# Optimization experiments

Measured on AMD Instinct MI355X. Metric: run time of the kernel, lower is better.

Reference implementation:

```python
import jax, jax.numpy as jnp
import numpy as np

# ---------------- Wigner-D machinery (real basis, e3nn conventions) ----------------

def _change_basis_real_to_complex(l):
    q = np.zeros((2*l+1, 2*l+1), dtype=np.complex128)
    for m in range(-l, 0):
        q[l+m, l+abs(m)] = 1/np.sqrt(2)
        q[l+m, l-abs(m)] = -1j/np.sqrt(2)
    q[l, l] = 1.0
    for m in range(1, l+1):
        q[l+m, l+abs(m)] = (-1)**m / np.sqrt(2)
        q[l+m, l-abs(m)] = 1j*(-1)**m / np.sqrt(2)
    return (-1j)**l * q

def _so3_generators(l):
    m = np.arange(-l, l)
    raising = np.diag(-np.sqrt(l*(l+1) - m*(m+1)), k=-1).astype(np.complex128)
    m = np.arange(-l+1, l+1)
    lowering = np.diag(np.sqrt(l*(l+1) - m*(m-1)), k=1).astype(np.complex128)
    m = np.arange(-l, l+1)
    Xs = [0.5*(raising+lowering), np.diag(1j*m), -0.5j*(raising-lowering)]
    Q = _change_basis_real_to_complex(l)
    return [np.real(np.conj(Q.T) @ X @ Q) for X in Xs]

def _expm_batch(A, t):
    # exp(t_n * A) for real antisymmetric A, via eigendecomposition
    w, V = np.linalg.eig(A.astype(np.complex128))
    Vinv = np.linalg.inv(V)
    E = np.exp(np.outer(t, w))  # [n, d]
    return np.real(np.einsum('ij,nj,jk->nik', V, E, Vinv))

def _wigner_D(l, alpha, beta, gamma):
    X = _so3_generators(l)
    return _expm_batch(X[1], alpha) @ _expm_batch(X[0], beta) @ _expm_batch(X[1], gamma)

def _flat_wigner(lmax, a, b, c):
    return np.concatenate([np.sqrt(2*l+1) * _wigner_D(l, a, b, c).reshape(len(a), -1)
                           for l in range(lmax+1)], axis=-1)

def _sh_alpha_beta(lmax, a, b):
    z = np.zeros_like(a)
    return np.concatenate([np.sqrt(2*l+1) * _wigner_D(l, a, b, z)[:, :, l]
                           for l in range(lmax+1)], axis=-1)

# ---------------- grids ----------------

def _so3_near_identity_grid(max_beta=np.pi/8, max_gamma=2*np.pi, n_alpha=8, n_beta=3, n_gamma=8):
    beta = np.arange(1, n_beta+1) * max_beta / n_beta
    alpha = np.linspace(0, 2*np.pi, n_alpha, endpoint=False)
    pre_gamma = np.linspace(-max_gamma, max_gamma, n_gamma)
    A, B, C = np.meshgrid(alpha, beta, pre_gamma, indexing='ij')
    return A.ravel(), B.ravel(), (C - A).ravel()

def _s2_near_identity_grid(max_beta=np.pi/8, n_alpha=8, n_beta=3):
    beta = np.arange(1, n_beta+1) * max_beta / n_beta
    alpha = np.linspace(0, 2*np.pi, n_alpha, endpoint=False)
    A, B = np.meshgrid(alpha, beta, indexing='ij')
    return A.ravel(), B.ravel()

def _so3_full_grid(res):
    a = 2*np.pi*np.arange(2*res)/(2*res)
    b = (np.arange(2*res)+0.5)*np.pi/(2*res)
    A, B, C = np.meshgrid(a, b, a, indexing='ij')
    qw = np.sin(B.ravel()); qw = qw / qw.sum()
    return A.ravel(), B.ravel(), C.ravel(), qw

# ---------------- constants for lmax=[6,4,4,2], feat=[32,64,128,128], N=8 ----------------
RES = 8
_ga, _gb, _gc = _so3_near_identity_grid()
D_K = jnp.asarray(_flat_wigner(4, _ga, _gb, _gc), jnp.float32)      # [192, 165] kernel basis
_fa, _fb, _fc, _qw = _so3_full_grid(RES)
D_ACT = jnp.asarray(_flat_wigner(4, _fa, _fb, _fc), jnp.float32)    # [4096, 165] act grid
QW = jnp.asarray(_qw, jnp.float32)                                   # [4096] quadrature
_sa, _sb = _s2_near_identity_grid()
Y_S2 = jnp.asarray(_sh_alpha_beta(2, _sa, _sb), jnp.float32)        # [24, 9]

# ---------------- layers ----------------

def _so3_linear(x, psi, lmax_in, lmax_out):
    # x: [B, f_in, sum_{l<=lmax_in}(2l+1)^2]; psi: [f_in, f_out, sum_{l<=lmin}(2l+1)^2]
    B, f_in, _ = x.shape
    f_out = psi.shape[1]
    lmin = min(lmax_in, lmax_out)
    outs, ox, op = [], 0, 0
    for l in range(lmax_out + 1):
        d = 2*l + 1
        if l <= lmin:
            xl = x[:, :, ox:ox + d*d].reshape(B, f_in, d, d)
            pl = psi[:, :, op:op + d*d].reshape(f_in, f_out, d, d)
            ol = jnp.einsum('xyuv,bxum->byvm', pl, xl) / np.sqrt(f_in * d)
            outs.append(ol.reshape(B, f_out, d*d))
            ox += d*d; op += d*d
        else:
            outs.append(jnp.zeros((B, f_out, d*d), x.dtype))
    return jnp.concatenate(outs, axis=-1)

def _so3_to_s2(x, psi, lmax_in, lmax_out):
    B, f_in, _ = x.shape
    f_out = psi.shape[1]
    lmin = min(lmax_in, lmax_out)
    outs, ox, op = [], 0, 0
    for l in range(lmax_out + 1):
        d = 2*l + 1
        if l <= lmin:
            xl = x[:, :, ox:ox + d*d].reshape(B, f_in, d, d)
            pl = psi[:, :, op:op + d].reshape(f_in, f_out, d)
            outs.append(jnp.einsum('xyu,bxum->bym', pl, xl) / np.sqrt(f_in * d))
            ox += d*d; op += d
        else:
            outs.append(jnp.zeros((B, f_out, d), x.dtype))
    return jnp.concatenate(outs, axis=-1)

def _so3_act(x):
    # SO3 Fourier -> grid signal, pointwise relu (2nd-moment normalized), grid -> Fourier
    s = jnp.einsum('ni,bfi->bfn', D_ACT, x)          # [B, f, 4096]
    s = np.sqrt(2.0) * jax.nn.relu(s)                 # normalize2mom(relu)
    return jnp.einsum('ni,bfn->bfi', D_ACT * QW[:, None], s)

def _forward(x, w0, w1, w_lin):
    n_k = D_K.shape[0]
    psi0 = jnp.einsum('ni,xyn->xyi', D_K, w0) / n_k   # [32, 64, 165]
    x = _so3_linear(x, psi0, 6, 4)
    x = _so3_act(x)
    psi1 = jnp.einsum('ni,xyn->xyi', D_K, w1) / n_k   # [64, 128, 165]
    x = _so3_linear(x, psi1, 4, 4)
    x = _so3_act(x)
    psi2 = jnp.einsum('ni,xyn->xyi', Y_S2, w_lin) / Y_S2.shape[0]  # [128, 128, 9]
    return _so3_to_s2(x, psi2, 4, 2)                  # [B, 128, 9]

# ---------------- harness ----------------

def setup_inputs() -> dict:
    key = jax.random.key(0)
    k1, k2, k3, k4 = jax.random.split(key, 4)
    return {
        'x': jax.random.normal(k1, (64, 32, 455), jnp.float32),
        'w0': jax.random.normal(k2, (32, 64, 192), jnp.float32),
        'w1': jax.random.normal(k3, (64, 128, 192), jnp.float32),
        'w_lin': jax.random.normal(k4, (128, 128, 24), jnp.float32),
    }

def reference(x, w0, w1, w_lin):
    return _forward(x, w0, w1, w_lin)
```

## Files before the change

kernel.cpp:

```cpp
#include <hip/hip_runtime.h>
#include <cmath>
#include <complex>
#include <cstring>
#include <vector>

#ifndef M_PI
#define M_PI 3.14159265358979323846
#endif

namespace wig {

using cplx = std::complex<double>;

static void matmul(const double* A, const double* B, double* C, int d) {
    for (int i = 0; i < d; ++i)
        for (int j = 0; j < d; ++j) {
            double s = 0;
            for (int k = 0; k < d; ++k) s += A[i*d+k]*B[k*d+j];
            C[i*d+j] = s;
        }
}

struct Gen { std::vector<double> X0, X1; int d; };

static Gen make_gen(int l) {
    int d = 2*l+1;
    std::vector<cplx> rais(d*d, cplx(0,0)), low(d*d, cplx(0,0));
    for (int i = 0; i+1 < d; ++i) {
        double m = -l + i;
        rais[(i+1)*d + i] = cplx(-std::sqrt(l*(l+1.0) - m*(m+1.0)), 0.0);
    }
    for (int i = 0; i+1 < d; ++i) {
        double m = -l + 1 + i;
        low[i*d + (i+1)] = cplx(std::sqrt(l*(l+1.0) - m*(m-1.0)), 0.0);
    }
    std::vector<cplx> Xc0(d*d, cplx(0,0)), Xc1(d*d, cplx(0,0));
    for (int i = 0; i < d*d; ++i) Xc0[i] = 0.5*(rais[i] + low[i]);
    for (int i = 0; i < d; ++i) Xc1[i*d+i] = cplx(0.0, (double)(-l + i));
    std::vector<cplx> q(d*d, cplx(0,0));
    double is2 = 1.0/std::sqrt(2.0);
    for (int m = -l; m < 0; ++m) {
        q[(l+m)*d + (l-m)] = cplx(is2, 0);
        q[(l+m)*d + (l+m)] = cplx(0, -is2);
    }
    q[l*d + l] = cplx(1,0);
    for (int m = 1; m <= l; ++m) {
        double sgn = (m & 1) ? -1.0 : 1.0;
        q[(l+m)*d + (l+m)] = cplx(sgn*is2, 0);
        q[(l+m)*d + (l-m)] = cplx(0, sgn*is2);
    }
    cplx f;
    switch (l & 3) { case 0: f = cplx(1,0); break; case 1: f = cplx(0,-1); break;
                     case 2: f = cplx(-1,0); break; default: f = cplx(0,1); break; }
    for (auto& v : q) v *= f;
    Gen g; g.d = d; g.X0.assign(d*d, 0.0); g.X1.assign(d*d, 0.0);
    const std::vector<cplx>* Xs[2] = {&Xc0, &Xc1};
    std::vector<double>* Xr[2] = {&g.X0, &g.X1};
    for (int a = 0; a < 2; ++a) {
        std::vector<cplx> t1(d*d, cplx(0,0)), t2(d*d, cplx(0,0));
        for (int i = 0; i < d; ++i)
            for (int k = 0; k < d; ++k) {
                cplx x = (*Xs[a])[i*d+k];
                if (x == cplx(0,0)) continue;
                for (int j = 0; j < d; ++j) t1[i*d+j] += x*q[k*d+j];
            }
        for (int k = 0; k < d; ++k)
            for (int i = 0; i < d; ++i) {
                cplx qc = std::conj(q[k*d+i]);
                if (qc == cplx(0,0)) continue;
                for (int j = 0; j < d; ++j) t2[i*d+j] += qc*t1[k*d+j];
            }
        for (int i = 0; i < d*d; ++i) (*Xr[a])[i] = t2[i].real();
    }
    return g;
}

static std::vector<double> expm_t(const std::vector<double>& A, int d, double t) {
    std::vector<double> M(d*d);
    for (int i = 0; i < d*d; ++i) M[i] = A[i]*t;
    double nrm = 0;
    for (int i = 0; i < d; ++i) {
        double rs = 0;
        for (int j = 0; j < d; ++j) rs += std::fabs(M[i*d+j]);
        if (rs > nrm) nrm = rs;
    }
    int sq = 0;
    while (nrm > 0.5) { nrm *= 0.5; ++sq; }
    double sc = std::ldexp(1.0, -sq);
    for (auto& v : M) v *= sc;
    std::vector<double> R(d*d, 0.0), T(d*d, 0.0), tmp(d*d);
    for (int i = 0; i < d; ++i) { R[i*d+i] = 1.0; T[i*d+i] = 1.0; }
    for (int k = 1; k <= 26; ++k) {
        matmul(T.data(), M.data(), tmp.data(), d);
        double inv = 1.0/(double)k;
        for (int i = 0; i < d*d; ++i) { T[i] = tmp[i]*inv; R[i] += T[i]; }
    }
    for (int s = 0; s < sq; ++s) { matmul(R.data(), R.data(), tmp.data(), d); R = tmp; }
    return R;
}

static std::vector<double> wigD(const Gen& g, double a, double b, double c) {
    auto Ea = expm_t(g.X1, g.d, a);
    auto Eb = expm_t(g.X0, g.d, b);
    auto Ec = expm_t(g.X1, g.d, c);
    std::vector<double> t(g.d*g.d), r(g.d*g.d);
    matmul(Ea.data(), Eb.data(), t.data(), g.d);
    matmul(t.data(), Ec.data(), r.data(), g.d);
    return r;
}

}

static inline unsigned short f2bf_h(float f) {
    unsigned u; std::memcpy(&u, &f, 4);
    unsigned r = (u + 0x7FFFu + ((u >> 16) & 1u)) >> 16;
    return (unsigned short)r;
}
static inline float bf2f_h(unsigned short s) {
    unsigned u = ((unsigned)s) << 16; float f; std::memcpy(&f, &u, 4); return f;
}
__device__ __forceinline__ unsigned short f2bf_d(float f) {
    unsigned u = __float_as_uint(f);
    return (unsigned short)((u + 0x7FFFu + ((u >> 16) & 1u)) >> 16);
}
__device__ __forceinline__ float bf2f_d(unsigned short s) {
    return __uint_as_float(((unsigned)s) << 16);
}

typedef short short8 __attribute__((ext_vector_type(8)));
typedef float f32x4 __attribute__((ext_vector_type(4)));

#define GLOAD_LDS16(g, l) \
    __builtin_amdgcn_global_load_lds( \
        (const __attribute__((address_space(1))) unsigned int*)(g), \
        (__attribute__((address_space(3))) unsigned int*)(l), 16, 0, 0)

static float*          g_QW   = nullptr;
static float*          g_YS2  = nullptr;
static unsigned short* g_DKS  = nullptr;
static unsigned short* g_B1   = nullptr;
static unsigned short* g_B2T  = nullptr;
static float*          g_scratch = nullptr;

static const size_t WS_OFF   = 0;
static const size_t AP_OFF   = WS_OFF + 2359296;
static const size_t BP_OFF   = AP_OFF + 1013760;
static const size_t A1_OFF   = BP_OFF + 2027520;
static const size_t GH_OFF   = A1_OFF + 2359296;
static const size_t GL_OFF   = GH_OFF + 16777216;
static const size_t PP_OFF   = GL_OFF + 16777216;
static const size_t ZB_OFF   = PP_OFF + 12582912;
static const size_t PSI2_OFF = ZB_OFF + 1572864;
static const size_t TOTAL_F  = PSI2_OFF + 147456;

namespace {
struct InitCtx {
    InitCtx() {
        using namespace wig;
        Gen gens[5];
        for (int l = 0; l <= 4; ++l) gens[l] = make_gen(l);
        const int loff[5] = {0, 1, 10, 35, 84};

        double alpha8[8], beta3[3], preg8[8];
        for (int i = 0; i < 8; ++i) alpha8[i] = 2.0*M_PI*i/8.0;
        for (int i = 0; i < 3; ++i) beta3[i] = (i+1)*(M_PI/8.0)/3.0;
        for (int i = 0; i < 8; ++i) preg8[i] = -2.0*M_PI + i*(4.0*M_PI/7.0);
        std::vector<float> hDK((size_t)192*165);
        for (int ia = 0; ia < 8; ++ia)
        for (int ib = 0; ib < 3; ++ib)
        for (int ic = 0; ic < 8; ++ic) {
            int n = ia*24 + ib*8 + ic;
            double a = alpha8[ia], b = beta3[ib], c = preg8[ic] - alpha8[ia];
            for (int l = 0; l <= 4; ++l) {
                int d = 2*l+1;
                auto Dl = wigD(gens[l], a, b, c);
                double s = std::sqrt(2.0*l+1.0);
                for (int e = 0; e < d*d; ++e)
                    hDK[(size_t)n*165 + loff[l] + e] = (float)(s*Dl[e]);
            }
        }

        double ag[16], bg[16];
        for (int i = 0; i < 16; ++i) ag[i] = 2.0*M_PI*i/16.0;
        for (int i = 0; i < 16; ++i) bg[i] = (i+0.5)*M_PI/16.0;
        std::vector<std::vector<double>> Ea[5], Eb[5];
        for (int l = 0; l <= 4; ++l) {
            Ea[l].resize(16); Eb[l].resize(16);
            for (int i = 0; i < 16; ++i) {
                Ea[l][i] = expm_t(gens[l].X1, gens[l].d, ag[i]);
                Eb[l][i] = expm_t(gens[l].X0, gens[l].d, bg[i]);
            }
        }
        double qsum = 0;
        for (int ib = 0; ib < 16; ++ib) qsum += std::sin(bg[ib]);
        qsum *= 256.0;
        std::vector<float> hDA((size_t)4096*165), hQW(4096);
        for (int ia = 0; ia < 16; ++ia)
        for (int ib = 0; ib < 16; ++ib) {
            for (int ic = 0; ic < 16; ++ic)
                hQW[ia*256 + ib*16 + ic] = (float)(std::sin(bg[ib]) / qsum);
            for (int l = 0; l <= 4; ++l) {
                int d = gens[l].d;
                std::vector<double> tAB((size_t)d*d), r((size_t)d*d);
                matmul(Ea[l][ia].data(), Eb[l][ib].data(), tAB.data(), d);
                double s = std::sqrt(2.0*l+1.0);
                for (int ic = 0; ic < 16; ++ic) {
                    int n = ia*256 + ib*16 + ic;
                    matmul(tAB.data(), Ea[l][ic].data(), r.data(), d);
                    for (int e = 0; e < d*d; ++e)
                        hDA[(size_t)n*165 + loff[l] + e] = (float)(s*r[e]);
                }
            }
        }

        const int l2off[3] = {0, 1, 4};
        std::vector<float> hY((size_t)24*9);
        for (int ia = 0; ia < 8; ++ia)
        for (int ib = 0; ib < 3; ++ib) {
            int n = ia*3 + ib;
            for (int l = 0; l <= 2; ++l) {
                int d = 2*l+1;
                auto Dl = wigD(gens[l], alpha8[ia], beta3[ib], 0.0);
                double s = std::sqrt(2.0*l+1.0);
                for (int u = 0; u < d; ++u)
                    hY[(size_t)n*9 + l2off[l] + u] = (float)(s*Dl[u*d + l]);
            }
        }

        std::vector<unsigned short> hDKS((size_t)192*576, 0);
        for (int i = 0; i < 165; ++i)
            for (int k = 0; k < 192; ++k) {
                float f = hDK[(size_t)k*165 + i];
                unsigned short h = f2bf_h(f);
                unsigned short lo = f2bf_h(f - bf2f_h(h));
                hDKS[(size_t)i*576 + k]       = h;
                hDKS[(size_t)i*576 + 192 + k] = lo;
                hDKS[(size_t)i*576 + 384 + k] = h;
            }

        std::vector<unsigned short> Dh((size_t)4096*192, 0), Dl2((size_t)4096*192, 0);
        for (int n = 0; n < 4096; ++n)
            for (int i = 0; i < 165; ++i) {
                float f = hDA[(size_t)n*165 + i];
                unsigned short h = f2bf_h(f);
                Dh[(size_t)n*192 + i] = h;
                Dl2[(size_t)n*192 + i] = f2bf_h(f - bf2f_h(h));
            }
        std::vector<unsigned short> hB1((size_t)4096*576);
        for (int n = 0; n < 4096; ++n)
            for (int j = 0; j < 192; ++j) {
                hB1[(size_t)n*576 + j]       = Dh[(size_t)n*192 + j];
                hB1[(size_t)n*576 + 192 + j] = Dl2[(size_t)n*192 + j];
                hB1[(size_t)n*576 + 384 + j] = Dh[(size_t)n*192 + j];
            }
        std::vector<unsigned short> hB2T((size_t)192*12288);
        for (int j = 0; j < 192; ++j)
            for (int k = 0; k < 4096; ++k) {
                hB2T[(size_t)j*12288 + k]        = Dh[(size_t)k*192 + j];
                hB2T[(size_t)j*12288 + 4096 + k] = Dl2[(size_t)k*192 + j];
                hB2T[(size_t)j*12288 + 8192 + k] = Dh[(size_t)k*192 + j];
            }

        (void)hipMalloc((void**)&g_QW,  hQW.size()*sizeof(float));
        (void)hipMalloc((void**)&g_YS2, hY.size()*sizeof(float));
        (void)hipMalloc((void**)&g_DKS, hDKS.size()*sizeof(unsigned short));
        (void)hipMalloc((void**)&g_B1,  hB1.size()*sizeof(unsigned short));
        (void)hipMalloc((void**)&g_B2T, hB2T.size()*sizeof(unsigned short));
        (void)hipMalloc((void**)&g_scratch, TOTAL_F*sizeof(float));
        (void)hipMemcpy(g_QW,  hQW.data(),  hQW.size()*sizeof(float),  hipMemcpyHostToDevice);
        (void)hipMemcpy(g_YS2, hY.data(),   hY.size()*sizeof(float),   hipMemcpyHostToDevice);
        (void)hipMemcpy(g_DKS, hDKS.data(), hDKS.size()*sizeof(unsigned short), hipMemcpyHostToDevice);
        (void)hipMemcpy(g_B1,  hB1.data(),  hB1.size()*sizeof(unsigned short),  hipMemcpyHostToDevice);
        (void)hipMemcpy(g_B2T, hB2T.data(), hB2T.size()*sizeof(unsigned short), hipMemcpyHostToDevice);
    }
};
static InitCtx g_init_ctx;
}

struct PsiArgs {
    const unsigned short* A;
    const unsigned short* B;
    unsigned short* O;
    int boff[5], kp[5];
    int fout;
};
struct APackArgs {
    const float* X;
    unsigned short* O;
    int cum[6];
    int aoff[5], kp[5], kl[5];
    int bs, fs, total;
};
struct LinArgs {
    const unsigned short* A;
    const unsigned short* B;
    unsigned short* O;
    int cum[6];
    int aoff[5], boff[5], kp[5];
    float rs[5];
    int fout;
};

__device__ __constant__ int c_loff[5] = {0, 1, 10, 35, 84};

__device__ __forceinline__ int swz_src8(int c) { return ((c ^ (c >> 3)) & 7) * 8; }


__global__ __launch_bounds__(256) void sph_psi2_kernel(
        const float* __restrict__ wl, const float* __restrict__ Y,
        float* __restrict__ psi2) {
    __shared__ float Ys[216];
    int tid = threadIdx.x;
    if (tid < 216) Ys[tid] = Y[tid];
    __syncthreads();
    int o = blockIdx.x*256 + tid;
    const float* w = wl + (size_t)o*24;
    float wv[24];
    #pragma unroll
    for (int k = 0; k < 24; k += 4) {
        f32x4 v = *(const f32x4*)&w[k];
        wv[k] = v[0]; wv[k+1] = v[1]; wv[k+2] = v[2]; wv[k+3] = v[3];
    }
    float acc[9] = {};
    #pragma unroll
    for (int k = 0; k < 24; ++k)
        #pragma unroll
        for (int i = 0; i < 9; ++i)
            acc[i] += wv[k] * Ys[k*9 + i];
    float* po = psi2 + (size_t)o*9;
    #pragma unroll
    for (int i = 0; i < 9; ++i) po[i] = acc[i] * (1.0f/24.0f);
}

__global__ __launch_bounds__(64) void sph_s2_wave(
        const float* __restrict__ z, const float* __restrict__ psi2,
        float* __restrict__ out) {
    int blk = blockIdx.x;
    int b = blk >> 7, y = blk & 127;
    int lane = threadIdx.x;
    float acc[9] = {};
    #pragma unroll
    for (int xi = 0; xi < 2; ++xi) {
        int x = lane + xi*64;
        const float* zr = z + (size_t)(b*128 + x)*192;
        const float* pr = psi2 + (size_t)(x*128 + y)*9;
        float p[9];
        #pragma unroll
        for (int i = 0; i < 9; ++i) p[i] = pr[i];
        acc[0] += p[0] * zr[0];
        #pragma unroll
        for (int u = 0; u < 3; ++u)
            #pragma unroll
            for (int m = 0; m < 3; ++m)
                acc[1+m] += p[1+u] * zr[1 + u*3 + m];
        #pragma unroll
        for (int u = 0; u < 5; ++u)
            #pragma unroll
            for (int m = 0; m < 5; ++m)
                acc[4+m] += p[4+u] * zr[10 + u*5 + m];
    }
    #pragma unroll
    for (int i = 0; i < 9; ++i) {
        float v = acc[i];
        #pragma unroll
        for (int off = 32; off > 0; off >>= 1)
            v += __shfl_down(v, off, 64);
        acc[i] = v;
    }
    if (lane == 0) {
        float* po = out + (size_t)blk*9;
        const float s0 = 0.0883883476483184406f;
        const float s1 = 0.0510310363079828938f;
        const float s2 = 0.0395284707521047416f;
        po[0] = acc[0] * s0;
        po[1] = acc[1] * s1; po[2] = acc[2] * s1; po[3] = acc[3] * s1;
        po[4] = acc[4] * s2; po[5] = acc[5] * s2; po[6] = acc[6] * s2;
        po[7] = acc[7] * s2; po[8] = acc[8] * s2;
    }
}

__global__ void sph_wpack_kernel(const float* __restrict__ w, unsigned short* __restrict__ o, int total) {
    int t = blockIdx.x*blockDim.x + threadIdx.x;
    if (t >= total) return;
    int row = t / 192, k = t % 192;
    float v = w[t];
    unsigned short hi = f2bf_d(v);
    unsigned short lo = f2bf_d(v - bf2f_d(hi));
    size_t b = (size_t)row*576 + k;
    o[b] = hi; o[b+192] = hi; o[b+384] = lo;
}

__global__ void sph_apack_kernel(APackArgs ar) {
    int t = blockIdx.x*blockDim.x + threadIdx.x;
    if (t >= ar.total) return;
    int l = 0;
    #pragma unroll
    for (int i = 1; i < 5; ++i) if (t >= ar.cum[i]) l = i;
    int e = t - ar.cum[l];
    int d = 2*l + 1;
    int K = ar.kl[l];
    int row = e / K, k = e % K;
    int b = row / d, m = row % d;
    int x = k / d, u = k % d;
    float v = ar.X[(size_t)b*ar.bs + (size_t)x*ar.fs + c_loff[l] + u*d + m];
    unsigned short hi = f2bf_d(v);
    unsigned short lo = f2bf_d(v - bf2f_d(hi));
    int kp = ar.kp[l];
    size_t base = (size_t)ar.aoff[l] + (size_t)row*(3*kp);
    ar.O[base + k] = hi; ar.O[base + kp + k] = hi; ar.O[base + 2*kp + k] = lo;
}

__global__ void sph_reduce_kernel(const float* __restrict__ Pp, float* __restrict__ z, int P) {
    int o = blockIdx.x*blockDim.x + threadIdx.x;
    if (o >= P*192) return;
    float s = 0.f;
    for (int zz = 0; zz < 8; ++zz) s += Pp[(size_t)zz*P*192 + o];
    z[o] = s;
}

__global__ __launch_bounds__(256) void sph_psi_mfma(PsiArgs ar, int M) {
    __shared__ __align__(16) unsigned short As[64*64];
    __shared__ __align__(16) unsigned short Bs[64*64];
    int tid = threadIdx.x, lane = tid & 63, wid = tid >> 6;
    int l15 = lane & 15, l4 = lane >> 4;
    int sw = l15 & 7;
    int bm = blockIdx.x * 64, bn = blockIdx.y * 64;
    f32x4 acc[4] = {};
    for (int k0 = 0; k0 < 576; k0 += 64) {
        #pragma unroll
        for (int i = 0; i < 2; ++i) {
            int c = tid + i*256;
            int row = c >> 3, kb = swz_src8(c);
            GLOAD_LDS16(ar.A + (size_t)(bm + row)*576 + k0 + kb, As + c*8);
            GLOAD_LDS16(ar.B + (size_t)(bn + row)*576 + k0 + kb, Bs + c*8);
        }
        __syncthreads();
        #pragma unroll
        for (int ks = 0; ks < 2; ++ks) {
            int cs = ((ks*4 + l4) ^ sw) * 8;
            short8 av = *(const short8*)&As[(wid*16 + l15)*64 + cs];
            #pragma unroll
            for (int nj = 0; nj < 4; ++nj) {
                short8 bv = *(const short8*)&Bs[(nj*16 + l15)*64 + cs];
                acc[nj] = __builtin_amdgcn_mfma_f32_16x16x32_bf16(av, bv, acc[nj], 0, 0, 0);
            }
        }
        __syncthreads();
    }
    #pragma unroll
    for (int nj = 0; nj < 4; ++nj) {
        int i = bn + nj*16 + l15;
        if (i >= 165) continue;
        int l, st;
        if (i < 1)       { l = 0; st = 0;  }
        else if (i < 10) { l = 1; st = 1;  }
        else if (i < 35) { l = 2; st = 10; }
        else if (i < 84) { l = 3; st = 35; }
        else             { l = 4; st = 84; }
        int d = 2*l + 1;
        int w = i - st;
        int u = w / d, v = w % d;
        int kp = ar.kp[l];
        #pragma unroll
        for (int r = 0; r < 4; ++r) {
            int R = bm + wid*16 + l4*4 + r;
            int x = R / ar.fout, y = R % ar.fout;
            float val = acc[nj][r] * (1.0f/192.0f);
            unsigned short hi = f2bf_d(val);
            unsigned short lo = f2bf_d(val - bf2f_d(hi));
            size_t base = (size_t)ar.boff[l] + (size_t)(y*d + v)*(3*kp) + (x*d + u);
            ar.O[base] = hi; ar.O[base + kp] = lo; ar.O[base + 2*kp] = hi;
        }
    }
}

__global__ __launch_bounds__(256) void sph_lin_mfma(LinArgs ar) {
    int bid = blockIdx.x;
    int l = 0;
    #pragma unroll
    for (int i = 1; i < 5; ++i) if (bid >= ar.cum[i]) l = i;
    int t = bid - ar.cum[l];
    int d = 2*l + 1;
    int NB = (ar.fout >> 6) * d;
    int tm = t / NB, tn = t % NB;
    int K3 = 3 * ar.kp[l];
    const unsigned short* Ab = ar.A + ar.aoff[l] + (size_t)tm*64*K3;
    const unsigned short* Bb = ar.B + ar.boff[l] + (size_t)tn*64*K3;
    __shared__ __align__(16) unsigned short As[64*64];
    __shared__ __align__(16) unsigned short Bs[64*64];
    int tid = threadIdx.x, lane = tid & 63, wid = tid >> 6;
    int l15 = lane & 15, l4 = lane >> 4;
    int sw = l15 & 7;
    f32x4 acc[4] = {};
    for (int k0 = 0; k0 < K3; k0 += 64) {
        #pragma unroll
        for (int i = 0; i < 2; ++i) {
            int c = tid + i*256;
            int row = c >> 3, kb = swz_src8(c);
            GLOAD_LDS16(Ab + (size_t)row*K3 + k0 + kb, As + c*8);
            GLOAD_LDS16(Bb + (size_t)row*K3 + k0 + kb, Bs + c*8);
        }
        __syncthreads();
        #pragma unroll
        for (int ks = 0; ks < 2; ++ks) {
            int cs = ((ks*4 + l4) ^ sw) * 8;
            short8 av = *(const short8*)&As[(wid*16 + l15)*64 + cs];
            #pragma unroll
            for (int nj = 0; nj < 4; ++nj) {
                short8 bv = *(const short8*)&Bs[(nj*16 + l15)*64 + cs];
                acc[nj] = __builtin_amdgcn_mfma_f32_16x16x32_bf16(av, bv, acc[nj], 0, 0, 0);
            }
        }
        __syncthreads();
    }
    float rs = ar.rs[l];
    #pragma unroll
    for (int nj = 0; nj < 4; ++nj) {
        int col = tn*64 + nj*16 + l15;
        int y = col / d, v = col % d;
        #pragma unroll
        for (int r = 0; r < 4; ++r) {
            int row = tm*64 + wid*16 + l4*4 + r;
            int b = row / d, m = row % d;
            float val = acc[nj][r] * rs;
            unsigned short hi = f2bf_d(val);
            unsigned short lo = f2bf_d(val - bf2f_d(hi));
            size_t p = (size_t)(b*ar.fout + y)*576 + c_loff[l] + v*d + m;
            ar.O[p] = hi; ar.O[p + 192] = hi; ar.O[p + 384] = lo;
        }
    }
}

__global__ __launch_bounds__(256) void sph_gemm1_mfma(
        const unsigned short* __restrict__ A, const unsigned short* __restrict__ B,
        const float* __restrict__ qw,
        unsigned short* __restrict__ Gh, unsigned short* __restrict__ Gl, int M) {
    constexpr int K = 576;
    __shared__ __align__(16) unsigned short As[128*64];
    __shared__ __align__(16) unsigned short Bs[128*64];
    int tid = threadIdx.x;
    int lane = tid & 63, wid = tid >> 6;
    int wm = wid >> 1, wn = wid & 1;
    int bm = blockIdx.x * 128, bn = blockIdx.y * 128;
    int l15 = lane & 15, l4 = lane >> 4;
    int sw = l15 & 7;
    f32x4 acc[4][4] = {};
    for (int k0 = 0; k0 < K; k0 += 64) {
        #pragma unroll
        for (int i = 0; i < 4; ++i) {
            int c = tid + i*256;
            int row = c >> 3, kb = swz_src8(c);
            GLOAD_LDS16(A + (size_t)(bm + row)*K + k0 + kb, As + c*8);
            GLOAD_LDS16(B + (size_t)(bn + row)*K + k0 + kb, Bs + c*8);
        }
        __syncthreads();
        #pragma unroll
        for (int ks = 0; ks < 2; ++ks) {
            int cs = ((ks*4 + l4) ^ sw) * 8;
            short8 av[4], bv[4];
            #pragma unroll
            for (int mi = 0; mi < 4; ++mi)
                av[mi] = *(const short8*)&As[(wm*64 + mi*16 + l15)*64 + cs];
            #pragma unroll
            for (int nj = 0; nj < 4; ++nj)
                bv[nj] = *(const short8*)&Bs[(wn*64 + nj*16 + l15)*64 + cs];
            #pragma unroll
            for (int mi = 0; mi < 4; ++mi)
                #pragma unroll
                for (int nj = 0; nj < 4; ++nj)
                    acc[mi][nj] = __builtin_amdgcn_mfma_f32_16x16x32_bf16(av[mi], bv[nj], acc[mi][nj], 0, 0, 0);
        }
        __syncthreads();
    }
    const float SQ2 = 1.41421356237309515f;
    #pragma unroll
    for (int mi = 0; mi < 4; ++mi) {
        #pragma unroll
        for (int nj = 0; nj < 4; ++nj) {
            int col = bn + wn*64 + nj*16 + l15;
            float q = qw[col] * SQ2;
            #pragma unroll
            for (int r = 0; r < 4; ++r) {
                int row = bm + wm*64 + mi*16 + l4*4 + r;
                float g = fmaxf(acc[mi][nj][r], 0.f) * q;
                unsigned short hi = f2bf_d(g);
                unsigned short lo = f2bf_d(g - bf2f_d(hi));
                size_t idx = (size_t)row*4096 + col;
                Gh[idx] = hi; Gl[idx] = lo;
            }
        }
    }
}

__global__ __launch_bounds__(256) void sph_gemm2_mfma(
        const unsigned short* __restrict__ Gh, const unsigned short* __restrict__ Gl,
        const unsigned short* __restrict__ B, float* __restrict__ Pp, int M) {
    __shared__ __align__(16) unsigned short As[128*64];
    __shared__ __align__(16) unsigned short Bs[64*64];
    int tid = threadIdx.x;
    int lane = tid & 63, wid = tid >> 6;
    int wm = wid >> 1, wn = wid & 1;
    int bm = blockIdx.x * 128, bn = blockIdx.y * 64;
    int zc = blockIdx.z;
    int l15 = lane & 15, l4 = lane >> 4;
    int sw = l15 & 7;
    f32x4 acc[4][2] = {};
    for (int t = 0; t < 24; ++t) {
        int kg = zc*1536 + t*64;
        int seg = kg >> 12;
        const unsigned short* Abase = (seg == 2) ? Gl : Gh;
        int koff = kg & 4095;
        #pragma unroll
        for (int i = 0; i < 4; ++i) {
            int c = tid + i*256;
            int row = c >> 3, kb = swz_src8(c);
            GLOAD_LDS16(Abase + (size_t)(bm + row)*4096 + koff + kb, As + c*8);
        }
        #pragma unroll
        for (int i = 0; i < 2; ++i) {
            int c = tid + i*256;
            int row = c >> 3, kb = swz_src8(c);
            GLOAD_LDS16(B + (size_t)(bn + row)*12288 + kg + kb, Bs + c*8);
        }
        __syncthreads();
        #pragma unroll
        for (int ks = 0; ks < 2; ++ks) {
            int cs = ((ks*4 + l4) ^ sw) * 8;
            short8 av[4], bv[2];
            #pragma unroll
            for (int mi = 0; mi < 4; ++mi)
                av[mi] = *(const short8*)&As[(wm*64 + mi*16 + l15)*64 + cs];
            #pragma unroll
            for (int nj = 0; nj < 2; ++nj)
                bv[nj] = *(const short8*)&Bs[(wn*32 + nj*16 + l15)*64 + cs];
            #pragma unroll
            for (int mi = 0; mi < 4; ++mi)
                #pragma unroll
                for (int nj = 0; nj < 2; ++nj)
                    acc[mi][nj] = __builtin_amdgcn_mfma_f32_16x16x32_bf16(av[mi], bv[nj], acc[mi][nj], 0, 0, 0);
        }
        __syncthreads();
    }
    #pragma unroll
    for (int mi = 0; mi < 4; ++mi)
        #pragma unroll
        for (int nj = 0; nj < 2; ++nj) {
            int col = bn + wn*32 + nj*16 + l15;
            #pragma unroll
            for (int r = 0; r < 4; ++r) {
                int row = bm + wm*64 + mi*16 + l4*4 + r;
                Pp[((size_t)zc*M + row)*192 + col] = acc[mi][nj][r];
            }
        }
}

extern "C" void kernel_launch(void* const* d_in, const int* in_sizes, int n_in,
                              void* d_out, int out_size, void* d_ws, size_t ws_size,
                              hipStream_t stream) {
    const float* x  = (const float*)d_in[0];
    const float* w0 = (const float*)d_in[1];
    const float* w1 = (const float*)d_in[2];
    const float* wl = (const float*)d_in[3];
    float* out = (float*)d_out;

    unsigned short* Wsplit = (unsigned short*)(g_scratch + WS_OFF);
    unsigned short* Apack  = (unsigned short*)(g_scratch + AP_OFF);
    unsigned short* Bpack  = (unsigned short*)(g_scratch + BP_OFF);
    unsigned short* A1     = (unsigned short*)(g_scratch + A1_OFF);
    unsigned short* Gh     = (unsigned short*)(g_scratch + GH_OFF);
    unsigned short* Gl     = (unsigned short*)(g_scratch + GL_OFF);
    float* Pp   = g_scratch + PP_OFF;
    float* zbuf = g_scratch + ZB_OFF;
    float* psi2 = g_scratch + PSI2_OFF;

    (void)hipMemsetAsync(g_scratch + AP_OFF, 0, (1013760 + 2027520 + 2359296)*sizeof(float), stream);

    PsiArgs ps0; APackArgs ap0; LinArgs ln0;
    {
        const int kp[5]   = {64, 128, 192, 256, 320};
        const int kl[5]   = {32, 96, 160, 224, 288};
        const int aoff[5] = {0, 12288, 86016, 270336, 614400};
        const int cumT[6] = {0, 1, 10, 35, 84, 165};
        const int cumE[6] = {0, 2048, 20480, 71680, 172032, 337920};
        ps0.A = Wsplit; ps0.B = g_DKS; ps0.O = Bpack; ps0.fout = 64;
        ap0.X = x; ap0.O = Apack; ap0.bs = 32*455; ap0.fs = 455; ap0.total = 337920;
        ln0.A = Apack; ln0.B = Bpack; ln0.O = A1; ln0.fout = 64;
        for (int l = 0; l < 5; ++l) {
            ps0.boff[l] = aoff[l]; ps0.kp[l] = kp[l];
            ap0.aoff[l] = aoff[l]; ap0.kp[l] = kp[l]; ap0.kl[l] = kl[l];
            ln0.aoff[l] = aoff[l]; ln0.boff[l] = aoff[l]; ln0.kp[l] = kp[l];
            ln0.rs[l] = 1.0f/sqrtf(32.0f*(2*l+1));
        }
        for (int i = 0; i < 6; ++i) { ap0.cum[i] = cumE[i]; ln0.cum[i] = cumT[i]; }
    }
    PsiArgs ps1; APackArgs ap1; LinArgs ln1;
    {
        const int kp[5]   = {64, 192, 320, 448, 576};
        const int aoff[5] = {0, 12288, 122880, 430080, 1032192};
        const int boff[5] = {0, 24576, 245760, 860160, 2064384};
        const int cumT[6] = {0, 2, 20, 70, 168, 330};
        const int cumE[6] = {0, 4096, 40960, 143360, 344064, 675840};
        ps1.A = Wsplit; ps1.B = g_DKS; ps1.O = Bpack; ps1.fout = 128;
        ap1.X = zbuf; ap1.O = Apack; ap1.bs = 64*192; ap1.fs = 192; ap1.total = 675840;
        ln1.A = Apack; ln1.B = Bpack; ln1.O = A1; ln1.fout = 128;
        for (int l = 0; l < 5; ++l) {
            ps1.boff[l] = boff[l]; ps1.kp[l] = kp[l];
            ap1.aoff[l] = aoff[l]; ap1.kp[l] = kp[l]; ap1.kl[l] = kp[l];
            ln1.aoff[l] = aoff[l]; ln1.boff[l] = boff[l]; ln1.kp[l] = kp[l];
            ln1.rs[l] = 1.0f/sqrtf(64.0f*(2*l+1));
        }
        for (int i = 0; i < 6; ++i) { ap1.cum[i] = cumE[i]; ln1.cum[i] = cumT[i]; }
    }

    sph_wpack_kernel<<<(2048*192 + 255)/256, 256, 0, stream>>>(w0, Wsplit, 2048*192);
    sph_psi_mfma<<<dim3(2048/64, 3), 256, 0, stream>>>(ps0, 2048);
    sph_apack_kernel<<<(337920 + 255)/256, 256, 0, stream>>>(ap0);
    sph_lin_mfma<<<165, 256, 0, stream>>>(ln0);
    sph_gemm1_mfma<<<dim3(4096/128, 4096/128), 256, 0, stream>>>(A1, g_B1, g_QW, Gh, Gl, 4096);
    sph_gemm2_mfma<<<dim3(4096/128, 3, 8), 256, 0, stream>>>(Gh, Gl, g_B2T, Pp, 4096);
    sph_reduce_kernel<<<(4096*192 + 255)/256, 256, 0, stream>>>(Pp, zbuf, 4096);
    sph_wpack_kernel<<<(8192*192 + 255)/256, 256, 0, stream>>>(w1, Wsplit, 8192*192);
    sph_psi_mfma<<<dim3(8192/64, 3), 256, 0, stream>>>(ps1, 8192);
    sph_apack_kernel<<<(675840 + 255)/256, 256, 0, stream>>>(ap1);
    sph_lin_mfma<<<330, 256, 0, stream>>>(ln1);
    sph_gemm1_mfma<<<dim3(8192/128, 4096/128), 256, 0, stream>>>(A1, g_B1, g_QW, Gh, Gl, 8192);
    sph_gemm2_mfma<<<dim3(8192/128, 3, 8), 256, 0, stream>>>(Gh, Gl, g_B2T, Pp, 8192);
    sph_reduce_kernel<<<(8192*192 + 255)/256, 256, 0, stream>>>(Pp, zbuf, 8192);
    sph_psi2_kernel<<<64, 256, 0, stream>>>(wl, g_YS2, psi2);
    sph_s2_wave<<<8192, 64, 0, stream>>>(zbuf, psi2, out);
}
```

Before: 441.1 us.

## Fuse S2 activation GEMMs keeping ReLU intermediate in shared memory

Result: slower. 874.6 us (+98.3%).

```diff
diff --git a/kernel.cpp b/kernel.cpp
--- a/kernel.cpp
+++ b/kernel.cpp
@@ -531,127 +531,116 @@
     }
 }
 
-__global__ __launch_bounds__(256) void sph_gemm1_mfma(
-        const unsigned short* __restrict__ A, const unsigned short* __restrict__ B,
-        const float* __restrict__ qw,
-        unsigned short* __restrict__ Gh, unsigned short* __restrict__ Gl, int M) {
-    constexpr int K = 576;
+__global__ __launch_bounds__(256) void sph_act_fused(
+        const unsigned short* __restrict__ A1, const unsigned short* __restrict__ B1,
+        const unsigned short* __restrict__ B2T, const float* __restrict__ qw,
+        float* __restrict__ Pp, int M) {
     __shared__ __align__(16) unsigned short As[128*64];
-    __shared__ __align__(16) unsigned short Bs[128*64];
-    int tid = threadIdx.x;
-    int lane = tid & 63, wid = tid >> 6;
+    __shared__ __align__(16) unsigned short Bs[64*64];
+    __shared__ __align__(16) unsigned short Gh[128*64];
+    __shared__ __align__(16) unsigned short Gl[128*64];
+    int tid = threadIdx.x, lane = tid & 63, wid = tid >> 6;
     int wm = wid >> 1, wn = wid & 1;
-    int bm = blockIdx.x * 128, bn = blockIdx.y * 128;
+    int bm = blockIdx.x * 128;
+    int cs = blockIdx.y * 512;
     int l15 = lane & 15, l4 = lane >> 4;
     int sw = l15 & 7;
-    f32x4 acc[4][4] = {};
-    for (int k0 = 0; k0 < K; k0 += 64) {
-        #pragma unroll
-        for (int i = 0; i < 4; ++i) {
-            int c = tid + i*256;
-            int row = c >> 3, kb = swz_src8(c);
-            GLOAD_LDS16(A + (size_t)(bm + row)*K + k0 + kb, As + c*8);
-            GLOAD_LDS16(B + (size_t)(bn + row)*K + k0 + kb, Bs + c*8);
-        }
-        __syncthreads();
-        #pragma unroll
-        for (int ks = 0; ks < 2; ++ks) {
-            int cs = ((ks*4 + l4) ^ sw) * 8;
-            short8 av[4], bv[4];
-            #pragma unroll
-            for (int mi = 0; mi < 4; ++mi)
-                av[mi] = *(const short8*)&As[(wm*64 + mi*16 + l15)*64 + cs];
-            #pragma unroll
-            for (int nj = 0; nj < 4; ++nj)
-                bv[nj] = *(const short8*)&Bs[(wn*64 + nj*16 + l15)*64 + cs];
-            #pragma unroll
-            for (int mi = 0; mi < 4; ++mi)
+    const float SQ2 = 1.41421356237309515f;
+
+    f32x4 acc2[2][12] = {};
+
+    for (int sub = 0; sub < 8; ++sub) {
+        int sc = cs + sub*64;
+        f32x4 acc[4][2] = {};
+        for (int k0 = 0; k0 < 576; k0 += 64) {
+            #pragma unroll
+            for (int i = 0; i < 4; ++i) {
+                int c = tid + i*256;
+                int row = c >> 3, kb = swz_src8(c);
+                GLOAD_LDS16(A1 + (size_t)(bm + row)*576 + k0 + kb, As + c*8);
+            }
+            #pragma unroll
+            for (int i = 0; i < 2; ++i) {
+                int c = tid + i*256;
+                int row = c >> 3, kb = swz_src8(c);
+                GLOAD_LDS16(B1 + (size_t)(sc + row)*576 + k0 + kb, Bs + c*8);
+            }
+            __syncthreads();
+            #pragma unroll
+            for (int ks = 0; ks < 2; ++ks) {
+                int cshift = ((ks*4 + l4) ^ sw) * 8;
+                short8 av[4], bv[2];
                 #pragma unroll
-                for (int nj = 0; nj < 4; ++nj)
-                    acc[mi][nj] = __builtin_amdgcn_mfma_f32_16x16x32_bf16(av[mi], bv[nj], acc[mi][nj], 0, 0, 0);
-        }
-        __syncthreads();
-    }
-    const float SQ2 = 1.41421356237309515f;
-    #pragma unroll
-    for (int mi = 0; mi < 4; ++mi) {
-        #pragma unroll
-        for (int nj = 0; nj < 4; ++nj) {
-            int col = bn + wn*64 + nj*16 + l15;
-            float q = qw[col] * SQ2;
-            #pragma unroll
-            for (int r = 0; r < 4; ++r) {
-                int row = bm + wm*64 + mi*16 + l4*4 + r;
-                float g = fmaxf(acc[mi][nj][r], 0.f) * q;
-                unsigned short hi = f2bf_d(g);
-                unsigned short lo = f2bf_d(g - bf2f_d(hi));
-                size_t idx = (size_t)row*4096 + col;
-                Gh[idx] = hi; Gl[idx] = lo;
-            }
-        }
-    }
-}
-
-__global__ __launch_bounds__(256) void sph_gemm2_mfma(
-        const unsigned short* __restrict__ Gh, const unsigned short* __restrict__ Gl,
-        const unsigned short* __restrict__ B, float* __restrict__ Pp, int M) {
-    __shared__ __align__(16) unsigned short As[128*64];
-    __shared__ __align__(16) unsigned short Bs[64*64];
-    int tid = threadIdx.x;
-    int lane = tid & 63, wid = tid >> 6;
-    int wm = wid >> 1, wn = wid & 1;
-    int bm = blockIdx.x * 128, bn = blockIdx.y * 64;
-    int zc = blockIdx.z;
-    int l15 = lane & 15, l4 = lane >> 4;
-    int sw = l15 & 7;
-    f32x4 acc[4][2] = {};
-    for (int t = 0; t < 24; ++t) {
-        int kg = zc*1536 + t*64;
-        int seg = kg >> 12;
-        const unsigned short* Abase = (seg == 2) ? Gl : Gh;
-        int koff = kg & 4095;
-        #pragma unroll
-        for (int i = 0; i < 4; ++i) {
-            int c = tid + i*256;
-            int row = c >> 3, kb = swz_src8(c);
-            GLOAD_LDS16(Abase + (size_t)(bm + row)*4096 + koff + kb, As + c*8);
-        }
-        #pragma unroll
-        for (int i = 0; i < 2; ++i) {
-            int c = tid + i*256;
-            int row = c >> 3, kb = swz_src8(c);
-            GLOAD_LDS16(B + (size_t)(bn + row)*12288 + kg + kb, Bs + c*8);
-        }
-        __syncthreads();
-        #pragma unroll
-        for (int ks = 0; ks < 2; ++ks) {
-            int cs = ((ks*4 + l4) ^ sw) * 8;
-            short8 av[4], bv[2];
-            #pragma unroll
-            for (int mi = 0; mi < 4; ++mi)
-                av[mi] = *(const short8*)&As[(wm*64 + mi*16 + l15)*64 + cs];
-            #pragma unroll
-            for (int nj = 0; nj < 2; ++nj)
-                bv[nj] = *(const short8*)&Bs[(wn*32 + nj*16 + l15)*64 + cs];
-            #pragma unroll
-            for (int mi = 0; mi < 4; ++mi)
+                for (int mi = 0; mi < 4; ++mi)
+                    av[mi] = *(const short8*)&As[(wm*64 + mi*16 + l15)*64 + cshift];
                 #pragma unroll
                 for (int nj = 0; nj < 2; ++nj)
-                    acc[mi][nj] = __builtin_amdgcn_mfma_f32_16x16x32_bf16(av[mi], bv[nj], acc[mi][nj], 0, 0, 0);
+                    bv[nj] = *(const short8*)&Bs[(wn*32 + nj*16 + l15)*64 + cshift];
+                #pragma unroll
+                for (int mi = 0; mi < 4; ++mi)
+                    #pragma unroll
+                    for (int nj = 0; nj < 2; ++nj)
+                        acc[mi][nj] = __builtin_amdgcn_mfma_f32_16x16x32_bf16(av[mi], bv[nj], acc[mi][nj], 0, 0, 0);
+            }
+            __syncthreads();
+        }
+        #pragma unroll
+        for (int nj = 0; nj < 2; ++nj) {
+            int colr = wn*32 + nj*16 + l15;
+            float q = qw[sc + colr] * SQ2;
+            int cb = colr >> 3, ce = colr & 7;
+            #pragma unroll
+            for (int mi = 0; mi < 4; ++mi) {
+                #pragma unroll
+                for (int r = 0; r < 4; ++r) {
+                    int row = wm*64 + mi*16 + l4*4 + r;
+                    float g = fmaxf(acc[mi][nj][r], 0.f) * q;
+                    unsigned short hi = f2bf_d(g);
+                    unsigned short lo = f2bf_d(g - bf2f_d(hi));
+                    int idx = row*64 + ((cb ^ (row & 7)) << 3) + ce;
+                    Gh[idx] = hi; Gl[idx] = lo;
+                }
+            }
         }
         __syncthreads();
-    }
-    #pragma unroll
-    for (int mi = 0; mi < 4; ++mi)
-        #pragma unroll
-        for (int nj = 0; nj < 2; ++nj) {
-            int col = bn + wn*32 + nj*16 + l15;
+        int r2 = wid * 32;
+        #pragma unroll
+        for (int seg = 0; seg < 3; ++seg) {
+            const unsigned short* Gs = (seg == 2) ? Gl : Gh;
+            const unsigned short* Bb = B2T + (size_t)seg*4096 + sc;
+            #pragma unroll
+            for (int kk = 0; kk < 2; ++kk) {
+                short8 a2[2];
+                #pragma unroll
+                for (int mi = 0; mi < 2; ++mi) {
+                    int row = r2 + mi*16 + l15;
+                    int gr = ((kk*4 + l4) ^ (l15 & 7)) * 8;
+                    a2[mi] = *(const short8*)&Gs[row*64 + gr];
+                }
+                size_t kb = (size_t)(kk*32 + l4*8);
+                #pragma unroll
+                for (int jn = 0; jn < 12; ++jn) {
+                    short8 b2 = *(const short8*)(Bb + (size_t)(jn*16 + l15)*12288 + kb);
+                    acc2[0][jn] = __builtin_amdgcn_mfma_f32_16x16x32_bf16(a2[0], b2, acc2[0][jn], 0, 0, 0);
+                    acc2[1][jn] = __builtin_amdgcn_mfma_f32_16x16x32_bf16(a2[1], b2, acc2[1][jn], 0, 0, 0);
+                }
+            }
+        }
+        __syncthreads();
+    }
+    int ns = blockIdx.y;
+    #pragma unroll
+    for (int jn = 0; jn < 12; ++jn) {
+        int col = jn*16 + l15;
+        #pragma unroll
+        for (int mi = 0; mi < 2; ++mi) {
             #pragma unroll
             for (int r = 0; r < 4; ++r) {
-                int row = bm + wm*64 + mi*16 + l4*4 + r;
-                Pp[((size_t)zc*M + row)*192 + col] = acc[mi][nj][r];
-            }
-        }
+                int row = bm + wid*32 + mi*16 + l4*4 + r;
+                Pp[((size_t)ns*M + row)*192 + col] = acc2[mi][jn][r];
+            }
+        }
+    }
 }
 
 extern "C" void kernel_launch(void* const* d_in, const int* in_sizes, int n_in,
@@ -667,8 +656,6 @@
     unsigned short* Apack  = (unsigned short*)(g_scratch + AP_OFF);
     unsigned short* Bpack  = (unsigned short*)(g_scratch + BP_OFF);
     unsigned short* A1     = (unsigned short*)(g_scratch + A1_OFF);
-    unsigned short* Gh     = (unsigned short*)(g_scratch + GH_OFF);
-    unsigned short* Gl     = (unsigned short*)(g_scratch + GL_OFF);
     float* Pp   = g_scratch + PP_OFF;
     float* zbuf = g_scratch + ZB_OFF;
     float* psi2 = g_scratch + PSI2_OFF;
@@ -716,15 +703,13 @@
     sph_psi_mfma<<<dim3(2048/64, 3), 256, 0, stream>>>(ps0, 2048);
     sph_apack_kernel<<<(337920 + 255)/256, 256, 0, stream>>>(ap0);
     sph_lin_mfma<<<165, 256, 0, stream>>>(ln0);
-    sph_gemm1_mfma<<<dim3(4096/128, 4096/128), 256, 0, stream>>>(A1, g_B1, g_QW, Gh, Gl, 4096);
-    sph_gemm2_mfma<<<dim3(4096/128, 3, 8), 256, 0, stream>>>(Gh, Gl, g_B2T, Pp, 4096);
+    sph_act_fused<<<dim3(4096/128, 8), 256, 0, stream>>>(A1, g_B1, g_B2T, g_QW, Pp, 4096);
     sph_reduce_kernel<<<(4096*192 + 255)/256, 256, 0, stream>>>(Pp, zbuf, 4096);
     sph_wpack_kernel<<<(8192*192 + 255)/256, 256, 0, stream>>>(w1, Wsplit, 8192*192);
     sph_psi_mfma<<<dim3(8192/64, 3), 256, 0, stream>>>(ps1, 8192);
     sph_apack_kernel<<<(675840 + 255)/256, 256, 0, stream>>>(ap1);
     sph_lin_mfma<<<330, 256, 0, stream>>>(ln1);
-    sph_gemm1_mfma<<<dim3(8192/128, 4096/128), 256, 0, stream>>>(A1, g_B1, g_QW, Gh, Gl, 8192);
-    sph_gemm2_mfma<<<dim3(8192/128, 3, 8), 256, 0, stream>>>(Gh, Gl, g_B2T, Pp, 8192);
+    sph_act_fused<<<dim3(8192/128, 8), 256, 0, stream>>>(A1, g_B1, g_B2T, g_QW, Pp, 8192);
     sph_reduce_kernel<<<(8192*192 + 255)/256, 256, 0, stream>>>(Pp, zbuf, 8192);
     sph_psi2_kernel<<<64, 256, 0, stream>>>(wl, g_YS2, psi2);
     sph_s2_wave<<<8192, 64, 0, stream>>>(zbuf, psi2, out);
```

## Restructure split-bf16 gemm2 to load hi/lo tiles once and cover full N per block

Applied to the files above, without the earlier changes.

Result: no change. 448.5 us (+1.7%).

```diff
diff --git a/kernel.cpp b/kernel.cpp
--- a/kernel.cpp
+++ b/kernel.cpp
@@ -253,12 +253,11 @@
                 hB1[(size_t)n*576 + 192 + j] = Dl2[(size_t)n*192 + j];
                 hB1[(size_t)n*576 + 384 + j] = Dh[(size_t)n*192 + j];
             }
-        std::vector<unsigned short> hB2T((size_t)192*12288);
+        std::vector<unsigned short> hB2T((size_t)192*8192);
         for (int j = 0; j < 192; ++j)
             for (int k = 0; k < 4096; ++k) {
-                hB2T[(size_t)j*12288 + k]        = Dh[(size_t)k*192 + j];
-                hB2T[(size_t)j*12288 + 4096 + k] = Dl2[(size_t)k*192 + j];
-                hB2T[(size_t)j*12288 + 8192 + k] = Dh[(size_t)k*192 + j];
+                hB2T[(size_t)j*8192 + k]        = Dh[(size_t)k*192 + j];
+                hB2T[(size_t)j*8192 + 4096 + k] = Dl2[(size_t)k*192 + j];
             }
 
         (void)hipMalloc((void**)&g_QW,  hQW.size()*sizeof(float));
@@ -410,11 +409,11 @@
     ar.O[base + k] = hi; ar.O[base + kp + k] = hi; ar.O[base + 2*kp + k] = lo;
 }
 
-__global__ void sph_reduce_kernel(const float* __restrict__ Pp, float* __restrict__ z, int P) {
+__global__ void sph_reduce_kernel(const float* __restrict__ Pp, float* __restrict__ z, int P, int KC) {
     int o = blockIdx.x*blockDim.x + threadIdx.x;
     if (o >= P*192) return;
     float s = 0.f;
-    for (int zz = 0; zz < 8; ++zz) s += Pp[(size_t)zz*P*192 + o];
+    for (int zz = 0; zz < KC; ++zz) s += Pp[(size_t)zz*P*192 + o];
     z[o] = s;
 }
 
@@ -594,64 +593,72 @@
 
 __global__ __launch_bounds__(256) void sph_gemm2_mfma(
         const unsigned short* __restrict__ Gh, const unsigned short* __restrict__ Gl,
-        const unsigned short* __restrict__ B, float* __restrict__ Pp, int M) {
-    __shared__ __align__(16) unsigned short As[128*64];
-    __shared__ __align__(16) unsigned short Bs[64*64];
-    int tid = threadIdx.x;
-    int lane = tid & 63, wid = tid >> 6;
-    int wm = wid >> 1, wn = wid & 1;
-    int bm = blockIdx.x * 128, bn = blockIdx.y * 64;
-    int zc = blockIdx.z;
+        const unsigned short* __restrict__ B2, float* __restrict__ Pp,
+        int M, int nslab) {
+    __shared__ __align__(16) unsigned short AsH[128*64];
+    __shared__ __align__(16) unsigned short AsL[128*64];
+    __shared__ __align__(16) unsigned short BsH[192*64];
+    __shared__ __align__(16) unsigned short BsL[192*64];
+    int tid = threadIdx.x, lane = tid & 63, wid = tid >> 6;
+    int bm = blockIdx.x * 128;
+    int zc = blockIdx.y;
     int l15 = lane & 15, l4 = lane >> 4;
     int sw = l15 & 7;
-    f32x4 acc[4][2] = {};
-    for (int t = 0; t < 24; ++t) {
-        int kg = zc*1536 + t*64;
-        int seg = kg >> 12;
-        const unsigned short* Abase = (seg == 2) ? Gl : Gh;
-        int koff = kg & 4095;
+    f32x4 acc2[2][12] = {};
+    int kbase = zc * nslab * 64;
+    for (int t = 0; t < nslab; ++t) {
+        int kp = kbase + t*64;
         #pragma unroll
         for (int i = 0; i < 4; ++i) {
             int c = tid + i*256;
             int row = c >> 3, kb = swz_src8(c);
-            GLOAD_LDS16(Abase + (size_t)(bm + row)*4096 + koff + kb, As + c*8);
-        }
-        #pragma unroll
-        for (int i = 0; i < 2; ++i) {
+            GLOAD_LDS16(Gh + (size_t)(bm + row)*4096 + kp + kb, AsH + c*8);
+            GLOAD_LDS16(Gl + (size_t)(bm + row)*4096 + kp + kb, AsL + c*8);
+        }
+        #pragma unroll
+        for (int i = 0; i < 6; ++i) {
             int c = tid + i*256;
             int row = c >> 3, kb = swz_src8(c);
-            GLOAD_LDS16(B + (size_t)(bn + row)*12288 + kg + kb, Bs + c*8);
+            GLOAD_LDS16(B2 + (size_t)row*8192 + kp + kb, BsH + c*8);
+            GLOAD_LDS16(B2 + (size_t)row*8192 + 4096 + kp + kb, BsL + c*8);
         }
         __syncthreads();
         #pragma unroll
-        for (int ks = 0; ks < 2; ++ks) {
-            int cs = ((ks*4 + l4) ^ sw) * 8;
-            short8 av[4], bv[2];
-            #pragma unroll
-            for (int mi = 0; mi < 4; ++mi)
-                av[mi] = *(const short8*)&As[(wm*64 + mi*16 + l15)*64 + cs];
-            #pragma unroll
-            for (int nj = 0; nj < 2; ++nj)
-                bv[nj] = *(const short8*)&Bs[(wn*32 + nj*16 + l15)*64 + cs];
-            #pragma unroll
-            for (int mi = 0; mi < 4; ++mi)
+        for (int kk = 0; kk < 2; ++kk) {
+            int cs = ((kk*4 + l4) ^ sw) * 8;
+            short8 ah[2], al[2];
+            #pragma unroll
+            for (int mi = 0; mi < 2; ++mi) {
+                int row = wid*32 + mi*16 + l15;
+                ah[mi] = *(const short8*)&AsH[row*64 + cs];
+                al[mi] = *(const short8*)&AsL[row*64 + cs];
+            }
+            #pragma unroll
+            for (int jn = 0; jn < 12; ++jn) {
+                int brow = jn*16 + l15;
+                short8 bh = *(const short8*)&BsH[brow*64 + cs];
+                short8 bl = *(const short8*)&BsL[brow*64 + cs];
                 #pragma unroll
-                for (int nj = 0; nj < 2; ++nj)
-                    acc[mi][nj] = __builtin_amdgcn_mfma_f32_16x16x32_bf16(av[mi], bv[nj], acc[mi][nj], 0, 0, 0);
+                for (int mi = 0; mi < 2; ++mi) {
+                    acc2[mi][jn] = __builtin_amdgcn_mfma_f32_16x16x32_bf16(ah[mi], bh, acc2[mi][jn], 0, 0, 0);
+                    acc2[mi][jn] = __builtin_amdgcn_mfma_f32_16x16x32_bf16(ah[mi], bl, acc2[mi][jn], 0, 0, 0);
+                    acc2[mi][jn] = __builtin_amdgcn_mfma_f32_16x16x32_bf16(al[mi], bh, acc2[mi][jn], 0, 0, 0);
+                }
+            }
         }
         __syncthreads();
     }
     #pragma unroll
-    for (int mi = 0; mi < 4; ++mi)
-        #pragma unroll
-        for (int nj = 0; nj < 2; ++nj) {
-            int col = bn + wn*32 + nj*16 + l15;
+    for (int jn = 0; jn < 12; ++jn) {
+        int col = jn*16 + l15;
+        #pragma unroll
+        for (int mi = 0; mi < 2; ++mi)
             #pragma unroll
             for (int r = 0; r < 4; ++r) {
-                int row = bm + wm*64 + mi*16 + l4*4 + r;
-                Pp[((size_t)zc*M + row)*192 + col] = acc[mi][nj][r];
-            }
-        }
+                int row = bm + wid*32 + mi*16 + l4*4 + r;
+                Pp[((size_t)zc*M + row)*192 + col] = acc2[mi][jn][r];
+            }
+    }
 }
 
 extern "C" void kernel_launch(void* const* d_in, const int* in_sizes, int n_in,
@@ -717,15 +724,15 @@
     sph_apack_kernel<<<(337920 + 255)/256, 256, 0, stream>>>(ap0);
     sph_lin_mfma<<<165, 256, 0, stream>>>(ln0);
     sph_gemm1_mfma<<<dim3(4096/128, 4096/128), 256, 0, stream>>>(A1, g_B1, g_QW, Gh, Gl, 4096);
-    sph_gemm2_mfma<<<dim3(4096/128, 3, 8), 256, 0, stream>>>(Gh, Gl, g_B2T, Pp, 4096);
-    sph_reduce_kernel<<<(4096*192 + 255)/256, 256, 0, stream>>>(Pp, zbuf, 4096);
+    sph_gemm2_mfma<<<dim3(4096/128, 16), 256, 0, stream>>>(Gh, Gl, g_B2T, Pp, 4096, 4);
+    sph_reduce_kernel<<<(4096*192 + 255)/256, 256, 0, stream>>>(Pp, zbuf, 4096, 16);
     sph_wpack_kernel<<<(8192*192 + 255)/256, 256, 0, stream>>>(w1, Wsplit, 8192*192);
     sph_psi_mfma<<<dim3(8192/64, 3), 256, 0, stream>>>(ps1, 8192);
     sph_apack_kernel<<<(675840 + 255)/256, 256, 0, stream>>>(ap1);
     sph_lin_mfma<<<330, 256, 0, stream>>>(ln1);
     sph_gemm1_mfma<<<dim3(8192/128, 4096/128), 256, 0, stream>>>(A1, g_B1, g_QW, Gh, Gl, 8192);
-    sph_gemm2_mfma<<<dim3(8192/128, 3, 8), 256, 0, stream>>>(Gh, Gl, g_B2T, Pp, 8192);
-    sph_reduce_kernel<<<(8192*192 + 255)/256, 256, 0, stream>>>(Pp, zbuf, 8192);
+    sph_gemm2_mfma<<<dim3(8192/128, 8), 256, 0, stream>>>(Gh, Gl, g_B2T, Pp, 8192, 8);
+    sph_reduce_kernel<<<(8192*192 + 255)/256, 256, 0, stream>>>(Pp, zbuf, 8192, 8);
     sph_psi2_kernel<<<64, 256, 0, stream>>>(wl, g_YS2, psi2);
     sph_s2_wave<<<8192, 64, 0, stream>>>(zbuf, psi2, out);
 }
```
